# Performance work log

Measured on AMD Instinct MI355X. Metric: run time of the kernel, lower is better.

The kernel has to match this reference:

```python
import jax, jax.numpy as jnp
import numpy as np

B, S, D, H = 128, 64, 512, 256  # batch, seq_len, model_dim, lstm hidden (=D//2)
VOCAB, SEL, MLPD, CLS = 32000, 128, 1024, 3


def setup_inputs() -> dict:
    key = jax.random.key(0)
    ks = jax.random.split(key, 10)
    sc = 0.02
    return {
        "sentences": jax.random.randint(ks[0], (B, S), 0, VOCAB),
        "transitions": jnp.zeros((B, 2 * S - 1), dtype=jnp.int32),  # unused by pyramid path
        "embed_table": jax.random.normal(ks[1], (VOCAB, D), jnp.float32) * sc,
        "comp_W": jax.random.normal(ks[2], (2 * H, 5 * H), jnp.float32) * sc,
        "comp_b": jnp.zeros((5 * H,), jnp.float32),
        "sel_W1": jax.random.normal(ks[3], (2 * D, SEL), jnp.float32) * sc,
        "sel_b1": jnp.zeros((SEL,), jnp.float32),
        "sel_W2": jax.random.normal(ks[4], (SEL, 1), jnp.float32) * sc,
        "sel_b2": jnp.zeros((1,), jnp.float32),
        "mlp_W0": jax.random.normal(ks[5], (D, MLPD), jnp.float32) * sc,
        "mlp_b0": jnp.zeros((MLPD,), jnp.float32),
        "mlp_W1": jax.random.normal(ks[6], (MLPD, MLPD), jnp.float32) * sc,
        "mlp_b1": jnp.zeros((MLPD,), jnp.float32),
        "mlp_Wout": jax.random.normal(ks[7], (MLPD, CLS), jnp.float32) * sc,
        "mlp_bout": jnp.zeros((CLS,), jnp.float32),
    }


def _tree_lstm(left, right, W, b):
    # left/right: [..., D] state vectors holding [h; c]
    h_l, c_l = left[..., :H], left[..., H:]
    h_r, c_r = right[..., :H], right[..., H:]
    gates = jnp.concatenate([h_l, h_r], axis=-1) @ W + b  # [..., 5H]
    i, fl, fr, u, o = jnp.split(gates, 5, axis=-1)
    c = (jax.nn.sigmoid(fl) * c_l + jax.nn.sigmoid(fr) * c_r
         + jax.nn.sigmoid(i) * jnp.tanh(u))
    h = jax.nn.sigmoid(o) * jnp.tanh(c)
    return jnp.concatenate([h, c], axis=-1)


def reference(sentences, transitions, embed_table, comp_W, comp_b,
              sel_W1, sel_b1, sel_W2, sel_b2,
              mlp_W0, mlp_b0, mlp_W1, mlp_b1, mlp_Wout, mlp_bout):
    # embed (context encoder = identity)
    states = embed_table[sentences]  # [B, S, D]
    # soft pyramid: seq_len-1 merge layers, each shrinking the row by 1
    for layer in range(S - 1, 0, -1):
        left = states[:, :-1]   # [B, layer, D]
        right = states[:, 1:]   # [B, layer, D]
        comp = _tree_lstm(left, right, comp_W, comp_b)  # [B, layer, D]
        sel_in = jnp.concatenate([left, right], axis=-1)  # [B, layer, 2D]
        hid = jnp.tanh(sel_in @ sel_W1 + sel_b1)
        logits = (hid @ sel_W2 + sel_b2)[..., 0]  # [B, layer]
        probs = jax.nn.softmax(logits, axis=1)
        cs = jnp.cumsum(probs, axis=1)
        copy_right = (cs - probs)[..., None]          # sum probs[:p]
        copy_left = (cs[:, -1:] - cs)[..., None]      # sum probs[p+1:]
        select = probs[..., None]
        states = copy_left * left + copy_right * right + select * comp
    h = states[:, 0]  # [B, D]
    # 2-layer MLP classifier (eval mode: no dropout, no LN)
    h1 = jax.nn.relu(h @ mlp_W0 + mlp_b0)
    h2 = jax.nn.relu(h1 @ mlp_W1 + mlp_b1)
    return h2 @ mlp_Wout + mlp_bout  # [B, CLS]
```

## Files before the change

### kernel.cpp

```cpp
#include <hip/hip_runtime.h>
#include <hip/hip_bf16.h>
#include <math.h>

#define B_ 128
#define S_ 64
#define D_ 512
#define H_ 256
#define SEL_ 128
#define MLPD_ 1024
#define CLS_ 3

typedef __attribute__((ext_vector_type(8))) short bf16x8;
typedef __attribute__((ext_vector_type(4))) float f32x4;

__device__ __forceinline__ float sigf(float x) { return 1.f / (1.f + expf(-x)); }

__device__ __forceinline__ ushort bf16r(float x) {
    uint u = __float_as_uint(x);
    return (ushort)((u + 0x7fffu + ((u >> 16) & 1u)) >> 16);
}
__device__ __forceinline__ float bf2f(ushort h) { return __uint_as_float(((uint)h) << 16); }

__device__ __forceinline__ int xcd_chunk(int bid, int nb) {
    int q = nb >> 3, r = nb & 7;
    int xcd = bid & 7, j = bid >> 3;
    return (xcd < r ? xcd * (q + 1) : r * (q + 1) + (xcd - r) * q) + j;
}

__global__ __launch_bounds__(256) void k_embed(const int* __restrict__ sent,
                                               const float* __restrict__ emb,
                                               ushort* __restrict__ oh,
                                               ushort* __restrict__ ol) {
    int idx = blockIdx.x * 256 + threadIdx.x;
    int row = idx >> 7;
    int k4 = (idx & 127) << 2;
    int tok = sent[row];
    float4 v = *(const float4*)(emb + (size_t)tok * D_ + k4);
    ushort4 h, l;
    h.x = bf16r(v.x); l.x = bf16r(v.x - bf2f(h.x));
    h.y = bf16r(v.y); l.y = bf16r(v.y - bf2f(h.y));
    h.z = bf16r(v.z); l.z = bf16r(v.z - bf2f(h.z));
    h.w = bf16r(v.w); l.w = bf16r(v.w - bf2f(h.w));
    *(ushort4*)(oh + (size_t)row * D_ + k4) = h;
    *(ushort4*)(ol + (size_t)row * D_ + k4) = l;
}

__global__ __launch_bounds__(256) void k_tsplit(const float* __restrict__ src,
                                                ushort* __restrict__ dh,
                                                ushort* __restrict__ dl,
                                                int K, int N) {
    __shared__ float t[64][65];
    int n0 = blockIdx.x * 64, k0 = blockIdx.y * 64;
    int tx = threadIdx.x & 63, ty = threadIdx.x >> 6;
    for (int i = ty; i < 64; i += 4)
        t[i][tx] = src[(size_t)(k0 + i) * N + n0 + tx];
    __syncthreads();
    for (int i = ty; i < 64; i += 4) {
        float v = t[tx][i];
        ushort h = bf16r(v);
        size_t o = (size_t)(n0 + i) * K + k0 + tx;
        dh[o] = h;
        dl[o] = bf16r(v - bf2f(h));
    }
}

__global__ __launch_bounds__(256) void k_selhid(const ushort* __restrict__ sh,
                                                const ushort* __restrict__ sl,
                                                const ushort* __restrict__ w1h,
                                                const ushort* __restrict__ w1l,
                                                const float* __restrict__ b1,
                                                float* __restrict__ hid,
                                                int N, int M, int cdiv) {
    __shared__ __align__(16) ushort sAm[2][64][40];
    __shared__ __align__(16) ushort sBm[2][64][40];
    __shared__ int rb[64];
    int w = xcd_chunk(blockIdx.x, gridDim.x);
    int cxb = w & 1, ry = w >> 1;
    int tid = threadIdx.x, l = tid & 63, wid = tid >> 6;
    int wm = wid >> 1, wn = wid & 1;
    int r0 = ry * 64;
    int c0b = cxb * 64;
    int lr = l & 15, lk = (l >> 4) << 3;

    if (tid < 64) {
        int g = r0 + tid;
        int q = (int)(((long long)g * cdiv) >> 20);
        rb[tid] = (g + q) * 512;
    }
    __syncthreads();

    float bias[2];
#pragma unroll
    for (int t = 0; t < 2; t++) bias[t] = b1[c0b + wn * 32 + t * 16 + lr];

    const ushort* aSrc[2]; ushort* aDst[2];
    const ushort* bSrc[2]; ushort* bDst[2];
#pragma unroll
    for (int i = 0; i < 2; i++) {
        int idx = tid + i * 256;
        int p = idx >> 8, rem = idx & 255;
        int r = rem >> 2, s = rem & 3;
        aSrc[i] = (p ? sl : sh) + rb[r] + s * 8;
        aDst[i] = &sAm[p][r][s * 8];
        bSrc[i] = (p ? w1l : w1h) + (c0b + r) * 1024 + s * 8;
        bDst[i] = &sBm[p][r][s * 8];
    }

    f32x4 z = {0.f, 0.f, 0.f, 0.f};
    f32x4 acc[2][2] = {{z, z}, {z, z}};
    bf16x8 gA[2], gB[2];

#define SSTAGE_LOAD(kk) do {                                               \
        _Pragma("unroll")                                                  \
        for (int i = 0; i < 2; i++) {                                      \
            gA[i] = *(const bf16x8*)(aSrc[i] + (kk));                      \
            gB[i] = *(const bf16x8*)(bSrc[i] + (kk));                      \
        }                                                                  \
    } while (0)
#define SSTAGE_WRITE() do {                                                \
        _Pragma("unroll")                                                  \
        for (int i = 0; i < 2; i++) {                                      \
            *(bf16x8*)aDst[i] = gA[i];                                     \
            *(bf16x8*)bDst[i] = gB[i];                                     \
        }                                                                  \
    } while (0)

    SSTAGE_LOAD(0);
    SSTAGE_WRITE();
    __syncthreads();

    for (int ks = 0; ks < 32; ks++) {
        if (ks < 31) SSTAGE_LOAD((ks + 1) * 32);
        bf16x8 fa[2][2], fb[2][2];
#pragma unroll
        for (int t = 0; t < 2; t++) {
            int ar = wm * 32 + t * 16 + lr;
            fa[0][t] = *(const bf16x8*)&sAm[0][ar][lk];
            fa[1][t] = *(const bf16x8*)&sAm[1][ar][lk];
            int bc = wn * 32 + t * 16 + lr;
            fb[0][t] = *(const bf16x8*)&sBm[0][bc][lk];
            fb[1][t] = *(const bf16x8*)&sBm[1][bc][lk];
        }
#pragma unroll
        for (int ti = 0; ti < 2; ti++)
#pragma unroll
            for (int tj = 0; tj < 2; tj++) {
                acc[ti][tj] = __builtin_amdgcn_mfma_f32_16x16x32_bf16(fa[0][ti], fb[0][tj], acc[ti][tj], 0, 0, 0);
                acc[ti][tj] = __builtin_amdgcn_mfma_f32_16x16x32_bf16(fa[0][ti], fb[1][tj], acc[ti][tj], 0, 0, 0);
                acc[ti][tj] = __builtin_amdgcn_mfma_f32_16x16x32_bf16(fa[1][ti], fb[0][tj], acc[ti][tj], 0, 0, 0);
            }
        __syncthreads();
        if (ks < 31) {
            SSTAGE_WRITE();
            __syncthreads();
        }
    }
#undef SSTAGE_LOAD
#undef SSTAGE_WRITE

#pragma unroll
    for (int ti = 0; ti < 2; ti++)
#pragma unroll
        for (int tj = 0; tj < 2; tj++)
#pragma unroll
            for (int r = 0; r < 4; r++) {
                int g = r0 + wm * 32 + ti * 16 + ((l >> 4) << 2) + r;
                int c = c0b + wn * 32 + tj * 16 + lr;
                hid[(size_t)g * 128 + c] = tanhf(acc[ti][tj][r] + bias[tj]);
            }
}

__global__ __launch_bounds__(64) void k_coef(const float* __restrict__ hid,
                                             const float* __restrict__ W2,
                                             const float* __restrict__ b2,
                                             float* __restrict__ coef, int N) {
    int b = blockIdx.x, j = threadIdx.x;
    float x = -1e30f;
    if (j < N) {
        const float4* hrow = (const float4*)(hid + ((size_t)b * N + j) * 128);
        const float4* w2v = (const float4*)W2;
        float acc = 0.f;
#pragma unroll
        for (int k = 0; k < 32; k++) {
            float4 hv = hrow[k];
            float4 wv = w2v[k];
            acc += hv.x * wv.x + hv.y * wv.y + hv.z * wv.z + hv.w * wv.w;
        }
        x = acc + b2[0];
    }
    float mx = x;
#pragma unroll
    for (int o = 32; o >= 1; o >>= 1) mx = fmaxf(mx, __shfl_xor(mx, o));
    float p = (j < N) ? expf(x - mx) : 0.f;
    float tot = p;
#pragma unroll
    for (int o = 32; o >= 1; o >>= 1) tot += __shfl_xor(tot, o);
    float cs = p;
#pragma unroll
    for (int o = 1; o < 64; o <<= 1) {
        float t = __shfl_up(cs, o);
        if (j >= o) cs += t;
    }
    float inv = 1.f / tot;
    float prob = p * inv;
    float csn = cs * inv;
    float cslast = __shfl(csn, N - 1);
    if (j < N) {
        int g = b * N + j;
        coef[g * 3 + 0] = cslast - csn;
        coef[g * 3 + 1] = csn - prob;
        coef[g * 3 + 2] = prob;
    }
}

__global__ __launch_bounds__(256) void k_compose(const ushort* __restrict__ sh,
                                                 const ushort* __restrict__ sl,
                                                 const ushort* __restrict__ wth,
                                                 const ushort* __restrict__ wtl,
                                                 const float* __restrict__ cbias,
                                                 const float* __restrict__ coef,
                                                 ushort* __restrict__ dh,
                                                 ushort* __restrict__ dl,
                                                 float* __restrict__ root,
                                                 int N, int M, int cdiv) {
    __shared__ __align__(16) ushort sAm[2][64][40];
    __shared__ __align__(16) ushort sBm[2][160][40];
    __shared__ int rb[64];
    int w = xcd_chunk(blockIdx.x, gridDim.x);
    int cx = w & 7, ry = w >> 3;
    int tid = threadIdx.x, l = tid & 63, wid = tid >> 6;
    int wm = wid >> 1, wn = wid & 1;
    int r0 = ry * 64;
    int cb_blk = cx * 32;
    int cbw = cb_blk + wn * 16;
    int lr = l & 15, lk = (l >> 4) << 3;

    if (tid < 64) {
        int g = r0 + tid;
        int q = (int)(((long long)g * cdiv) >> 20);
        rb[tid] = (g + q) * 512;
    }
    __syncthreads();

    float bias[5];
#pragma unroll
    for (int gt = 0; gt < 5; gt++) bias[gt] = cbias[gt * 256 + cbw + lr];

    const ushort* aSrc[2]; ushort* aDst[2];
#pragma unroll
    for (int i = 0; i < 2; i++) {
        int idx = tid + i * 256;
        int p = idx >> 8, rem = idx & 255;
        int r = rem >> 2, s = rem & 3;
        aSrc[i] = (p ? sl : sh) + rb[r] + s * 8;
        aDst[i] = &sAm[p][r][s * 8];
    }
    const ushort* bSrc[5]; ushort* bDst[5];
#pragma unroll
    for (int j = 0; j < 5; j++) {
        int idx = tid + j * 256;
        int p = (idx >= 640) ? 1 : 0;
        int rem = idx - p * 640;
        int br = rem >> 2, s = rem & 3;
        int col = (br >> 5) * 256 + cb_blk + (br & 31);
        bSrc[j] = (p ? wtl : wth) + col * 512 + s * 8;
        bDst[j] = &sBm[p][br][s * 8];
    }

    f32x4 z = {0.f, 0.f, 0.f, 0.f};
    f32x4 acc[2][5] = {{z, z, z, z, z}, {z, z, z, z, z}};
    bf16x8 gA[2], gB[5];

#define CSTAGE_LOAD(kk) do {                                               \
        int koff_ = ((kk) < 256) ? (kk) : (kk) + 256;                      \
        _Pragma("unroll")                                                  \
        for (int i = 0; i < 2; i++) gA[i] = *(const bf16x8*)(aSrc[i] + koff_); \
        _Pragma("unroll")                                                  \
        for (int j = 0; j < 5; j++) gB[j] = *(const bf16x8*)(bSrc[j] + (kk)); \
    } while (0)
#define CSTAGE_WRITE() do {                                                \
        _Pragma("unroll")                                                  \
        for (int i = 0; i < 2; i++) *(bf16x8*)aDst[i] = gA[i];             \
        _Pragma("unroll")                                                  \
        for (int j = 0; j < 5; j++) *(bf16x8*)bDst[j] = gB[j];             \
    } while (0)

    CSTAGE_LOAD(0);
    CSTAGE_WRITE();
    __syncthreads();

    for (int ks = 0; ks < 16; ks++) {
        if (ks < 15) CSTAGE_LOAD((ks + 1) * 32);
        bf16x8 fa[2][2], fb[2][5];
#pragma unroll
        for (int t = 0; t < 2; t++) {
            int ar = wm * 32 + t * 16 + lr;
            fa[0][t] = *(const bf16x8*)&sAm[0][ar][lk];
            fa[1][t] = *(const bf16x8*)&sAm[1][ar][lk];
        }
#pragma unroll
        for (int gt = 0; gt < 5; gt++) {
            int br = gt * 32 + wn * 16 + lr;
            fb[0][gt] = *(const bf16x8*)&sBm[0][br][lk];
            fb[1][gt] = *(const bf16x8*)&sBm[1][br][lk];
        }
#pragma unroll
        for (int gt = 0; gt < 5; gt++)
#pragma unroll
            for (int t = 0; t < 2; t++) {
                acc[t][gt] = __builtin_amdgcn_mfma_f32_16x16x32_bf16(fa[0][t], fb[0][gt], acc[t][gt], 0, 0, 0);
                acc[t][gt] = __builtin_amdgcn_mfma_f32_16x16x32_bf16(fa[0][t], fb[1][gt], acc[t][gt], 0, 0, 0);
                acc[t][gt] = __builtin_amdgcn_mfma_f32_16x16x32_bf16(fa[1][t], fb[0][gt], acc[t][gt], 0, 0, 0);
            }
        __syncthreads();
        if (ks < 15) {
            CSTAGE_WRITE();
            __syncthreads();
        }
    }
#undef CSTAGE_LOAD
#undef CSTAGE_WRITE

#pragma unroll
    for (int t = 0; t < 2; t++)
#pragma unroll
        for (int r = 0; r < 4; r++) {
            int lrow = wm * 32 + t * 16 + ((l >> 4) << 2) + r;
            int m = r0 + lrow;
            size_t sb = (size_t)rb[lrow];
            int c = cbw + lr;
            float cl = coef[m * 3 + 0], cr = coef[m * 3 + 1], sel = coef[m * 3 + 2];
            float h_l = bf2f(sh[sb + c])       + bf2f(sl[sb + c]);
            float c_l = bf2f(sh[sb + 256 + c]) + bf2f(sl[sb + 256 + c]);
            float h_r = bf2f(sh[sb + 512 + c]) + bf2f(sl[sb + 512 + c]);
            float c_r = bf2f(sh[sb + 768 + c]) + bf2f(sl[sb + 768 + c]);
            float gi  = acc[t][0][r] + bias[0];
            float gfl = acc[t][1][r] + bias[1];
            float gfr = acc[t][2][r] + bias[2];
            float gu  = acc[t][3][r] + bias[3];
            float go  = acc[t][4][r] + bias[4];
            float cn = sigf(gfl) * c_l + sigf(gfr) * c_r + sigf(gi) * tanhf(gu);
            float hn = sigf(go) * tanhf(cn);
            float oh = cl * h_l + cr * h_r + sel * hn;
            float oc = cl * c_l + cr * c_r + sel * cn;
            size_t ob = (size_t)m * 512 + c;
            ushort hh = bf16r(oh);
            dh[ob] = hh;
            dl[ob] = bf16r(oh - bf2f(hh));
            ushort hc = bf16r(oc);
            dh[ob + 256] = hc;
            dl[ob + 256] = bf16r(oc - bf2f(hc));
            if (N == 1) {
                root[ob] = oh;
                root[ob + 256] = oc;
            }
        }
}

template <int ACT>
__global__ __launch_bounds__(256) void k_gemm(const float* __restrict__ A,
                                              const float* __restrict__ W,
                                              const float* __restrict__ bias,
                                              float* __restrict__ C,
                                              int M, int K, int Nc) {
    __shared__ float Xs[32][36];
    __shared__ float Ws[32][64];
    int tid = threadIdx.x;
    int r0 = blockIdx.x * 32, c0 = blockIdx.y * 64;
    int ct = tid & 15, rt = tid >> 4;
    float acc[2][4];
#pragma unroll
    for (int r = 0; r < 2; r++)
#pragma unroll
        for (int q = 0; q < 4; q++) {
            int c = c0 + ct * 4 + q;
            acc[r][q] = (c < Nc) ? bias[c] : 0.f;
        }
    for (int kk = 0; kk < K; kk += 32) {
        __syncthreads();
        {
            int m = tid >> 3, k4 = (tid & 7) << 2;
            float4 v = {0.f, 0.f, 0.f, 0.f};
            if (r0 + m < M) v = *(const float4*)(A + (size_t)(r0 + m) * K + kk + k4);
            Xs[k4 + 0][m] = v.x; Xs[k4 + 1][m] = v.y; Xs[k4 + 2][m] = v.z; Xs[k4 + 3][m] = v.w;
        }
#pragma unroll
        for (int i = 0; i < 2; i++) {
            int idx = tid + i * 256;
            int k = idx >> 4, c4 = (idx & 15) << 2;
            int c = c0 + c4;
            float4 v = {0.f, 0.f, 0.f, 0.f};
            if (c + 3 < Nc) {
                v = *(const float4*)(W + (size_t)(kk + k) * Nc + c);
            } else {
                float tmp[4] = {0.f, 0.f, 0.f, 0.f};
                for (int j = 0; j < 4; j++)
                    if (c + j < Nc) tmp[j] = W[(size_t)(kk + k) * Nc + c + j];
                v = *(float4*)tmp;
            }
            *(float4*)&Ws[k][c4] = v;
        }
        __syncthreads();
#pragma unroll
        for (int k = 0; k < 32; k++) {
            float x0 = Xs[k][rt * 2], x1 = Xs[k][rt * 2 + 1];
            float wv[4];
            *(float4*)wv = *(const float4*)&Ws[k][ct * 4];
#pragma unroll
            for (int q = 0; q < 4; q++) { acc[0][q] += x0 * wv[q]; acc[1][q] += x1 * wv[q]; }
        }
    }
#pragma unroll
    for (int r = 0; r < 2; r++) {
        int g = r0 + rt * 2 + r;
        if (g >= M) continue;
#pragma unroll
        for (int q = 0; q < 4; q++) {
            int c = c0 + ct * 4 + q;
            if (c >= Nc) continue;
            float v = acc[r][q];
            if (ACT == 1) v = fmaxf(v, 0.f);
            C[(size_t)g * Nc + c] = v;
        }
    }
}

extern "C" void kernel_launch(void* const* d_in, const int* in_sizes, int n_in,
                              void* d_out, int out_size, void* d_ws, size_t ws_size,
                              hipStream_t stream) {
    const int*   sent     = (const int*)d_in[0];
    const float* emb      = (const float*)d_in[2];
    const float* comp_W   = (const float*)d_in[3];
    const float* comp_b   = (const float*)d_in[4];
    const float* sel_W1   = (const float*)d_in[5];
    const float* sel_b1   = (const float*)d_in[6];
    const float* sel_W2   = (const float*)d_in[7];
    const float* sel_b2   = (const float*)d_in[8];
    const float* mlp_W0   = (const float*)d_in[9];
    const float* mlp_b0   = (const float*)d_in[10];
    const float* mlp_W1   = (const float*)d_in[11];
    const float* mlp_b1   = (const float*)d_in[12];
    const float* mlp_Wout = (const float*)d_in[13];
    const float* mlp_bout = (const float*)d_in[14];
    float* outp = (float*)d_out;

    char* p = (char*)d_ws;
    ushort* sh0  = (ushort*)p; p += (size_t)B_ * S_ * D_ * 2;
    ushort* sl0  = (ushort*)p; p += (size_t)B_ * S_ * D_ * 2;
    ushort* sh1  = (ushort*)p; p += (size_t)B_ * S_ * D_ * 2;
    ushort* sl1  = (ushort*)p; p += (size_t)B_ * S_ * D_ * 2;
    ushort* wth  = (ushort*)p; p += (size_t)1280 * 512 * 2;
    ushort* wtl  = (ushort*)p; p += (size_t)1280 * 512 * 2;
    ushort* w1th = (ushort*)p; p += (size_t)128 * 1024 * 2;
    ushort* w1tl = (ushort*)p; p += (size_t)128 * 1024 * 2;
    float*  hid  = (float*)p;  p += (size_t)B_ * 63 * SEL_ * 4;
    float*  coef = (float*)p;  p += (size_t)B_ * 63 * 3 * 4;
    float*  root = (float*)p;  p += (size_t)B_ * D_ * 4;
    float*  h1   = (float*)p;  p += (size_t)B_ * MLPD_ * 4;
    float*  h2   = (float*)p;  p += (size_t)B_ * MLPD_ * 4;

    k_embed<<<dim3(4096), dim3(256), 0, stream>>>(sent, emb, sh0, sl0);
    k_tsplit<<<dim3(20, 8), dim3(256), 0, stream>>>(comp_W, wth, wtl, 512, 1280);
    k_tsplit<<<dim3(2, 16), dim3(256), 0, stream>>>(sel_W1, w1th, w1tl, 1024, 128);

    ushort* shs = sh0; ushort* sls = sl0;
    ushort* shd = sh1; ushort* sld = sl1;
    for (int L = S_; L >= 2; --L) {
        int N = L - 1;
        int M = B_ * N;
        int cdiv = (1048576 + N - 1) / N;
        k_selhid<<<dim3(2 * (M / 64)), dim3(256), 0, stream>>>(shs, sls, w1th, w1tl, sel_b1, hid, N, M, cdiv);
        k_coef<<<dim3(B_), dim3(64), 0, stream>>>(hid, sel_W2, sel_b2, coef, N);
        k_compose<<<dim3(8 * (M / 64)), dim3(256), 0, stream>>>(shs, sls, wth, wtl, comp_b, coef,
                                                                shd, sld, root, N, M, cdiv);
        ushort* th = shs; shs = shd; shd = th;
        ushort* tl = sls; sls = sld; sld = tl;
    }

    k_gemm<1><<<dim3(4, 16), dim3(256), 0, stream>>>(root, mlp_W0, mlp_b0, h1, B_, 512, MLPD_);
    k_gemm<1><<<dim3(4, 16), dim3(256), 0, stream>>>(h1, mlp_W1, mlp_b1, h2, B_, 1024, MLPD_);
    k_gemm<0><<<dim3(4, 1), dim3(256), 0, stream>>>(h2, mlp_Wout, mlp_bout, outp, B_, 1024, CLS_);
}
```

Measured before the change: 3.878 ms.

## Fuse selector W2 dot into selector GEMM and softmax into compose kernel

The selector GEMM now covers all 128 hidden columns per block and reduces tanh(hid)·W2 in-register with shuffles and shared memory, writing only one logit per row instead of the full hidden matrix. The separate softmax/cumsum kernel is removed; each compose block loads the logits for the batches it touches and computes its own copy/select coefficients in shared memory. This drops one launch per layer (63 layers) and the hidden-matrix round-trip, at the cost of half as many selector blocks and redundant serial softmax work per compose block.

```diff
diff --git a/kernel.cpp b/kernel.cpp
--- a/kernel.cpp
+++ b/kernel.cpp
@@ -64,22 +64,23 @@
     }
 }
 
-__global__ __launch_bounds__(256) void k_selhid(const ushort* __restrict__ sh,
-                                                const ushort* __restrict__ sl,
-                                                const ushort* __restrict__ w1h,
-                                                const ushort* __restrict__ w1l,
-                                                const float* __restrict__ b1,
-                                                float* __restrict__ hid,
-                                                int N, int M, int cdiv) {
+__global__ __launch_bounds__(256) void k_sellogit(const ushort* __restrict__ sh,
+                                                  const ushort* __restrict__ sl,
+                                                  const ushort* __restrict__ w1h,
+                                                  const ushort* __restrict__ w1l,
+                                                  const float* __restrict__ b1,
+                                                  const float* __restrict__ W2,
+                                                  const float* __restrict__ b2,
+                                                  float* __restrict__ logits,
+                                                  int N, int M, int cdiv) {
     __shared__ __align__(16) ushort sAm[2][64][40];
-    __shared__ __align__(16) ushort sBm[2][64][40];
+    __shared__ __align__(16) ushort sBm[2][128][40];
     __shared__ int rb[64];
+    __shared__ float lpart[2][64];
     int w = xcd_chunk(blockIdx.x, gridDim.x);
-    int cxb = w & 1, ry = w >> 1;
+    int r0 = w * 64;
     int tid = threadIdx.x, l = tid & 63, wid = tid >> 6;
     int wm = wid >> 1, wn = wid & 1;
-    int r0 = ry * 64;
-    int c0b = cxb * 64;
     int lr = l & 15, lk = (l >> 4) << 3;
 
     if (tid < 64) {
@@ -89,12 +90,15 @@
     }
     __syncthreads();
 
-    float bias[2];
-#pragma unroll
-    for (int t = 0; t < 2; t++) bias[t] = b1[c0b + wn * 32 + t * 16 + lr];
+    float bias[4], w2v[4];
+#pragma unroll
+    for (int tj = 0; tj < 4; tj++) {
+        int c = wn * 64 + tj * 16 + lr;
+        bias[tj] = b1[c];
+        w2v[tj] = W2[c];
+    }
 
     const ushort* aSrc[2]; ushort* aDst[2];
-    const ushort* bSrc[2]; ushort* bDst[2];
 #pragma unroll
     for (int i = 0; i < 2; i++) {
         int idx = tid + i * 256;
@@ -102,27 +106,33 @@
         int r = rem >> 2, s = rem & 3;
         aSrc[i] = (p ? sl : sh) + rb[r] + s * 8;
         aDst[i] = &sAm[p][r][s * 8];
-        bSrc[i] = (p ? w1l : w1h) + (c0b + r) * 1024 + s * 8;
-        bDst[i] = &sBm[p][r][s * 8];
+    }
+    const ushort* bSrc[4]; ushort* bDst[4];
+#pragma unroll
+    for (int j = 0; j < 4; j++) {
+        int idx = tid + j * 256;
+        int p = (idx >= 512) ? 1 : 0;
+        int rem = idx - p * 512;
+        int br = rem >> 2, s = rem & 3;
+        bSrc[j] = (p ? w1l : w1h) + br * 1024 + s * 8;
+        bDst[j] = &sBm[p][br][s * 8];
     }
 
     f32x4 z = {0.f, 0.f, 0.f, 0.f};
-    f32x4 acc[2][2] = {{z, z}, {z, z}};
-    bf16x8 gA[2], gB[2];
+    f32x4 acc[2][4] = {{z, z, z, z}, {z, z, z, z}};
+    bf16x8 gA[2], gB[4];
 
 #define SSTAGE_LOAD(kk) do {                                               \
         _Pragma("unroll")                                                  \
-        for (int i = 0; i < 2; i++) {                                      \
-            gA[i] = *(const bf16x8*)(aSrc[i] + (kk));                      \
-            gB[i] = *(const bf16x8*)(bSrc[i] + (kk));                      \
-        }                                                                  \
+        for (int i = 0; i < 2; i++) gA[i] = *(const bf16x8*)(aSrc[i] + (kk)); \
+        _Pragma("unroll")                                                  \
+        for (int j = 0; j < 4; j++) gB[j] = *(const bf16x8*)(bSrc[j] + (kk)); \
     } while (0)
 #define SSTAGE_WRITE() do {                                                \
         _Pragma("unroll")                                                  \
-        for (int i = 0; i < 2; i++) {                                      \
-            *(bf16x8*)aDst[i] = gA[i];                                     \
-            *(bf16x8*)bDst[i] = gB[i];                                     \
-        }                                                                  \
+        for (int i = 0; i < 2; i++) *(bf16x8*)aDst[i] = gA[i];             \
+        _Pragma("unroll")                                                  \
+        for (int j = 0; j < 4; j++) *(bf16x8*)bDst[j] = gB[j];             \
     } while (0)
 
     SSTAGE_LOAD(0);
@@ -131,20 +141,23 @@
 
     for (int ks = 0; ks < 32; ks++) {
         if (ks < 31) SSTAGE_LOAD((ks + 1) * 32);
-        bf16x8 fa[2][2], fb[2][2];
+        bf16x8 fa[2][2], fb[2][4];
 #pragma unroll
         for (int t = 0; t < 2; t++) {
             int ar = wm * 32 + t * 16 + lr;
             fa[0][t] = *(const bf16x8*)&sAm[0][ar][lk];
             fa[1][t] = *(const bf16x8*)&sAm[1][ar][lk];
-            int bc = wn * 32 + t * 16 + lr;
-            fb[0][t] = *(const bf16x8*)&sBm[0][bc][lk];
-            fb[1][t] = *(const bf16x8*)&sBm[1][bc][lk];
+        }
+#pragma unroll
+        for (int tj = 0; tj < 4; tj++) {
+            int bc = wn * 64 + tj * 16 + lr;
+            fb[0][tj] = *(const bf16x8*)&sBm[0][bc][lk];
+            fb[1][tj] = *(const bf16x8*)&sBm[1][bc][lk];
         }
 #pragma unroll
         for (int ti = 0; ti < 2; ti++)
 #pragma unroll
-            for (int tj = 0; tj < 2; tj++) {
+            for (int tj = 0; tj < 4; tj++) {
                 acc[ti][tj] = __builtin_amdgcn_mfma_f32_16x16x32_bf16(fa[0][ti], fb[0][tj], acc[ti][tj], 0, 0, 0);
                 acc[ti][tj] = __builtin_amdgcn_mfma_f32_16x16x32_bf16(fa[0][ti], fb[1][tj], acc[ti][tj], 0, 0, 0);
                 acc[ti][tj] = __builtin_amdgcn_mfma_f32_16x16x32_bf16(fa[1][ti], fb[0][tj], acc[ti][tj], 0, 0, 0);
@@ -158,58 +171,35 @@
 #undef SSTAGE_LOAD
 #undef SSTAGE_WRITE
 
+    float part[2][4];
 #pragma unroll
     for (int ti = 0; ti < 2; ti++)
 #pragma unroll
-        for (int tj = 0; tj < 2; tj++)
-#pragma unroll
-            for (int r = 0; r < 4; r++) {
-                int g = r0 + wm * 32 + ti * 16 + ((l >> 4) << 2) + r;
-                int c = c0b + wn * 32 + tj * 16 + lr;
-                hid[(size_t)g * 128 + c] = tanhf(acc[ti][tj][r] + bias[tj]);
-            }
-}
-
-__global__ __launch_bounds__(64) void k_coef(const float* __restrict__ hid,
-                                             const float* __restrict__ W2,
-                                             const float* __restrict__ b2,
-                                             float* __restrict__ coef, int N) {
-    int b = blockIdx.x, j = threadIdx.x;
-    float x = -1e30f;
-    if (j < N) {
-        const float4* hrow = (const float4*)(hid + ((size_t)b * N + j) * 128);
-        const float4* w2v = (const float4*)W2;
-        float acc = 0.f;
-#pragma unroll
-        for (int k = 0; k < 32; k++) {
-            float4 hv = hrow[k];
-            float4 wv = w2v[k];
-            acc += hv.x * wv.x + hv.y * wv.y + hv.z * wv.z + hv.w * wv.w;
-        }
-        x = acc + b2[0];
-    }
-    float mx = x;
-#pragma unroll
-    for (int o = 32; o >= 1; o >>= 1) mx = fmaxf(mx, __shfl_xor(mx, o));
-    float p = (j < N) ? expf(x - mx) : 0.f;
-    float tot = p;
-#pragma unroll
-    for (int o = 32; o >= 1; o >>= 1) tot += __shfl_xor(tot, o);
-    float cs = p;
-#pragma unroll
-    for (int o = 1; o < 64; o <<= 1) {
-        float t = __shfl_up(cs, o);
-        if (j >= o) cs += t;
-    }
-    float inv = 1.f / tot;
-    float prob = p * inv;
-    float csn = cs * inv;
-    float cslast = __shfl(csn, N - 1);
-    if (j < N) {
-        int g = b * N + j;
-        coef[g * 3 + 0] = cslast - csn;
-        coef[g * 3 + 1] = csn - prob;
-        coef[g * 3 + 2] = prob;
+        for (int r = 0; r < 4; r++) {
+            float s = 0.f;
+#pragma unroll
+            for (int tj = 0; tj < 4; tj++)
+                s += tanhf(acc[ti][tj][r] + bias[tj]) * w2v[tj];
+            part[ti][r] = s;
+        }
+#pragma unroll
+    for (int off = 1; off < 16; off <<= 1)
+#pragma unroll
+        for (int ti = 0; ti < 2; ti++)
+#pragma unroll
+            for (int r = 0; r < 4; r++)
+                part[ti][r] += __shfl_xor(part[ti][r], off);
+    if ((l & 15) == 0) {
+#pragma unroll
+        for (int ti = 0; ti < 2; ti++)
+#pragma unroll
+            for (int r = 0; r < 4; r++)
+                lpart[wn][wm * 32 + ti * 16 + ((l >> 4) << 2) + r] = part[ti][r];
+    }
+    __syncthreads();
+    if (tid < 64) {
+        int g = r0 + tid;
+        logits[g] = lpart[0][tid] + lpart[1][tid] + b2[0];
     }
 }
 
@@ -218,7 +208,7 @@
                                                  const ushort* __restrict__ wth,
                                                  const ushort* __restrict__ wtl,
                                                  const float* __restrict__ cbias,
-                                                 const float* __restrict__ coef,
+                                                 const float* __restrict__ logits,
                                                  ushort* __restrict__ dh,
                                                  ushort* __restrict__ dl,
                                                  float* __restrict__ root,
@@ -226,6 +216,8 @@
     __shared__ __align__(16) ushort sAm[2][64][40];
     __shared__ __align__(16) ushort sBm[2][160][40];
     __shared__ int rb[64];
+    __shared__ float slog[192];
+    __shared__ float scoef[64][3];
     int w = xcd_chunk(blockIdx.x, gridDim.x);
     int cx = w & 7, ry = w >> 3;
     int tid = threadIdx.x, l = tid & 63, wid = tid >> 6;
@@ -235,12 +227,36 @@
     int cbw = cb_blk + wn * 16;
     int lr = l & 15, lk = (l >> 4) << 3;
 
+    int blo = (int)(((long long)r0 * cdiv) >> 20);
+    int bhi = (int)(((long long)(r0 + 63) * cdiv) >> 20);
+    int cnt = (bhi - blo + 1) * N;
     if (tid < 64) {
         int g = r0 + tid;
         int q = (int)(((long long)g * cdiv) >> 20);
         rb[tid] = (g + q) * 512;
     }
-    __syncthreads();
+    if (tid < cnt) slog[tid] = logits[blo * N + tid];
+    __syncthreads();
+
+    if (tid < 64) {
+        int g = r0 + tid;
+        int b = (int)(((long long)g * cdiv) >> 20);
+        int j = g - b * N;
+        int o = (b - blo) * N;
+        float mx = -1e30f;
+        for (int k = 0; k < N; k++) mx = fmaxf(mx, slog[o + k]);
+        float tot = 0.f, cs = 0.f, pj = 0.f;
+        for (int k = 0; k < N; k++) {
+            float e = expf(slog[o + k] - mx);
+            tot += e;
+            if (k <= j) cs += e;
+            if (k == j) pj = e;
+        }
+        float inv = 1.f / tot;
+        scoef[tid][0] = (tot - cs) * inv;
+        scoef[tid][1] = (cs - pj) * inv;
+        scoef[tid][2] = pj * inv;
+    }
 
     float bias[5];
 #pragma unroll
@@ -329,7 +345,7 @@
             int m = r0 + lrow;
             size_t sb = (size_t)rb[lrow];
             int c = cbw + lr;
-            float cl = coef[m * 3 + 0], cr = coef[m * 3 + 1], sel = coef[m * 3 + 2];
+            float cl = scoef[lrow][0], cr = scoef[lrow][1], sel = scoef[lrow][2];
             float h_l = bf2f(sh[sb + c])       + bf2f(sl[sb + c]);
             float c_l = bf2f(sh[sb + 256 + c]) + bf2f(sl[sb + 256 + c]);
             float h_r = bf2f(sh[sb + 512 + c]) + bf2f(sl[sb + 512 + c]);
@@ -453,8 +469,7 @@
     ushort* wtl  = (ushort*)p; p += (size_t)1280 * 512 * 2;
     ushort* w1th = (ushort*)p; p += (size_t)128 * 1024 * 2;
     ushort* w1tl = (ushort*)p; p += (size_t)128 * 1024 * 2;
-    float*  hid  = (float*)p;  p += (size_t)B_ * 63 * SEL_ * 4;
-    float*  coef = (float*)p;  p += (size_t)B_ * 63 * 3 * 4;
+    float*  logits = (float*)p; p += (size_t)B_ * 63 * 4;
     float*  root = (float*)p;  p += (size_t)B_ * D_ * 4;
     float*  h1   = (float*)p;  p += (size_t)B_ * MLPD_ * 4;
     float*  h2   = (float*)p;  p += (size_t)B_ * MLPD_ * 4;
@@ -469,9 +484,9 @@
         int N = L - 1;
         int M = B_ * N;
         int cdiv = (1048576 + N - 1) / N;
-        k_selhid<<<dim3(2 * (M / 64)), dim3(256), 0, stream>>>(shs, sls, w1th, w1tl, sel_b1, hid, N, M, cdiv);
-        k_coef<<<dim3(B_), dim3(64), 0, stream>>>(hid, sel_W2, sel_b2, coef, N);
-        k_compose<<<dim3(8 * (M / 64)), dim3(256), 0, stream>>>(shs, sls, wth, wtl, comp_b, coef,
+        k_sellogit<<<dim3(M / 64), dim3(256), 0, stream>>>(shs, sls, w1th, w1tl, sel_b1,
+                                                           sel_W2, sel_b2, logits, N, M, cdiv);
+        k_compose<<<dim3(8 * (M / 64)), dim3(256), 0, stream>>>(shs, sls, wth, wtl, comp_b, logits,
                                                                 shd, sld, root, N, M, cdiv);
         ushort* th = shs; shs = shd; shd = th;
         ushort* tl = sls; sls = sld; sld = tl;
```

After: 4.145 ms. 1.07x slower.
